# Kernel tuning notes

Hardware: AMD Instinct MI355X
Metric: run time of the kernel (lower is better)

The kernel has to match this reference:

```python
import jax, jax.numpy as jnp
import numpy as np

B, G, C, H, ZD, K, P = 2048, 2000, 50, 256, 32, 10, 4


def _xavier(key, shape, fan_in, fan_out):
    std = (2.0 / (fan_in + fan_out)) ** 0.5
    return std * jax.random.normal(key, shape, dtype=jnp.float32)


def setup_inputs() -> dict:
    key = jax.random.key(0)
    ks = jax.random.split(key, 13)
    X = jax.random.normal(ks[0], (B, G), dtype=jnp.float32)
    M = (jax.random.uniform(ks[1], (C, G)) < 0.1).astype(jnp.float32)
    # backbone: Linear(G,H) + LeakyReLU + Linear(H,H) + LeakyReLU (n_layer_enc=2)
    W1 = _xavier(ks[2], (G, H), G, H)
    b1 = jnp.zeros((H,), dtype=jnp.float32)
    W2 = _xavier(ks[3], (H, H), H, H)
    b2 = jnp.zeros((H,), dtype=jnp.float32)
    # MultiChannelLinear: w [C, ZD, H], b [1, C, ZD] (kaiming-uniform-ish init)
    bound_w = (6.0 / H) ** 0.5
    cw = jax.random.uniform(ks[4], (C, ZD, H), minval=-bound_w, maxval=bound_w, dtype=jnp.float32)
    bound_b = 1.0 / (H ** 0.5)
    cb = jax.random.uniform(ks[5], (1, C, ZD), minval=-bound_b, maxval=bound_b, dtype=jnp.float32)
    prototypes = _xavier(ks[6], (C, K, P, ZD), P * ZD, K)
    logvar = _xavier(ks[7], (C, K, P), P, K)
    c_bias = jnp.zeros((C, K), dtype=jnp.float32)
    bias = jnp.zeros((K,), dtype=jnp.float32)
    importance = _xavier(ks[8], (1, C), C, 1)
    return {"X": X, "M": M, "W1": W1, "b1": b1, "W2": W2, "b2": b2,
            "cw": cw, "cb": cb, "prototypes": prototypes, "logvar": logvar,
            "c_bias": c_bias, "bias": bias, "importance": importance}


def reference(X, M, W1, b1, W2, b2, cw, cb, prototypes, logvar, c_bias, bias, importance):
    # encode: mask input per concept, run shared MLP backbone, per-concept heads
    xm = X[:, None, :] * M[None]                       # [B, C, G]
    h = jax.nn.leaky_relu(jnp.einsum('bcg,gh->bch', xm, W1) + b1)
    h = jax.nn.leaky_relu(jnp.einsum('bch,hk->bck', h, W2) + b2)
    Z = jnp.einsum('bch,coh->bco', h, cw) + cb          # [B, C, ZD]
    # importance scores (dropout p=0 -> identity)
    imp = jnp.abs(importance)                           # [1, C]
    # broadcast squared distance to prototypes: [B, C, K, P]
    diff = Z[:, :, None, None, :] - prototypes[None]
    c2p_dist_sq = jnp.sum(diff * diff, axis=-1)
    scaled = c2p_dist_sq / (2.0 * jnp.exp(logvar))[None]
    c_logits = -jnp.min(scaled, axis=-1) + c_bias[None]  # [B, C, K]
    logits = jnp.log(jnp.sum(jnp.exp(c_logits) * imp[0][None, :, None] + 1e-16, axis=1)) + bias[None]
    return logits, c_logits
```

## Files before the change

### kernel.cpp

```cpp
#include <hip/hip_runtime.h>
#include <hip/hip_bf16.h>

#define NB   2048
#define NG   2000
#define NC   50
#define NH   256
#define NZD  32
#define NK   10
#define NP   4
#define BT   64
#define GS   2048
#define KP   320
#define NCH  10

typedef short short8  __attribute__((ext_vector_type(8)));
typedef short short4v __attribute__((ext_vector_type(4)));
typedef float f32x4   __attribute__((ext_vector_type(4)));
typedef unsigned int uint2v __attribute__((ext_vector_type(2)));

__device__ __forceinline__ unsigned short f2bf(float f) {
    union { float f; unsigned u; } v; v.f = f;
    unsigned r = v.u + 0x7fffu + ((v.u >> 16) & 1u);
    return (unsigned short)(r >> 16);
}

__device__ __forceinline__ unsigned cvt_pk_bf16(float lo, float hi) {
    unsigned r;
    asm("v_cvt_pk_bf16_f32 %0, %1, %2" : "=v"(r) : "v"(lo), "v"(hi));
    return r;
}

__device__ __forceinline__ void gld16(const unsigned short* g, char* l) {
    __builtin_amdgcn_global_load_lds(
        (const __attribute__((address_space(1))) unsigned int*)g,
        (__attribute__((address_space(3))) unsigned int*)l, 16, 0, 0);
}

__global__ void build_gidx(const float* __restrict__ M, int* __restrict__ gidx,
                           int* __restrict__ gcnt) {
    int c = blockIdx.x;
    int t = threadIdx.x;
    __shared__ int wcnt[16];
    __shared__ int base;
    if (t == 0) base = 0;
    __syncthreads();
    for (int g0 = 0; g0 < NG; g0 += 1024) {
        int g = g0 + t;
        bool a = (g < NG) && (M[c * NG + g] != 0.0f);
        unsigned long long mask = __ballot(a);
        int lane = t & 63;
        int w = t >> 6;
        if (lane == 0) wcnt[w] = __popcll(mask);
        int pre = __popcll(mask & ((1ull << lane) - 1ull));
        __syncthreads();
        int woff = base;
        for (int i = 0; i < w; ++i) woff += wcnt[i];
        if (a) gidx[c * GS + woff + pre] = g;
        int tot = 0;
        #pragma unroll
        for (int i = 0; i < 16; ++i) tot += wcnt[i];
        __syncthreads();
        if (t == 0) base += tot;
        __syncthreads();
    }
    if (t == 0) gcnt[c] = base;
}

__global__ void prep_all(const float* __restrict__ X, const float* __restrict__ W1,
                         const float* __restrict__ W2, const float* __restrict__ cw,
                         const int* __restrict__ gidx, const int* __restrict__ gcnt,
                         unsigned short* __restrict__ xt, unsigned short* __restrict__ w1s,
                         unsigned short* __restrict__ w2s, unsigned short* __restrict__ cwb) {
    __shared__ float tile[64][65];
    const int bx = blockIdx.x;
    const int t  = threadIdx.x;
    if (bx < 1024) {
        int gb = bx & 31, bb = bx >> 5;
        int tx = t & 63, tq = t >> 6;
        #pragma unroll
        for (int i = 0; i < 16; ++i) {
            int r = tq * 16 + i;
            int gene = gb * 64 + tx;
            tile[r][tx] = (gene < NG) ? X[(size_t)(bb * 64 + r) * NG + gene] : 0.f;
        }
        __syncthreads();
        #pragma unroll
        for (int i = 0; i < 16; ++i) {
            int gl = tq * 16 + i;
            int gene = gb * 64 + gl;
            if (gene < NG)
                xt[(size_t)gene * NB + bb * 64 + tx] = f2bf(tile[tx][gl]);
        }
    } else if (bx < 1524) {
        int idx = bx - 1024;
        int ch = idx % NCH, c = idx / NCH;
        int col = t;
        int cnt = gcnt[c]; if (cnt > KP) cnt = KP;
        unsigned short v[32];
        #pragma unroll
        for (int kin = 0; kin < 32; ++kin) {
            int k = ch * 32 + kin;
            float x = 0.f;
            if (k < cnt) {
                int g = gidx[c * GS + k];
                x = W1[(size_t)g * NH + col];
            }
            v[kin] = f2bf(x);
        }
        unsigned short* dst = w1s + (((size_t)(c * NCH + ch)) * 256 + col) * 32;
        #pragma unroll
        for (int q = 0; q < 4; ++q) {
            short8 v8;
            #pragma unroll
            for (int i = 0; i < 8; ++i) v8[i] = (short)v[q * 8 + i];
            *(short8*)(dst + (q ^ ((col >> 1) & 3)) * 8) = v8;
        }
    } else if (bx < 1532) {
        int ch = bx - 1524;
        int col = t;
        unsigned short v[32];
        #pragma unroll
        for (int kin = 0; kin < 32; ++kin)
            v[kin] = f2bf(W2[(size_t)(ch * 32 + kin) * NH + col]);
        unsigned short* dst = w2s + ((size_t)ch * 256 + col) * 32;
        #pragma unroll
        for (int q = 0; q < 4; ++q) {
            short8 v8;
            #pragma unroll
            for (int i = 0; i < 8; ++i) v8[i] = (short)v[q * 8 + i];
            *(short8*)(dst + (q ^ ((col >> 1) & 3)) * 8) = v8;
        }
    } else {
        int c = bx - 1532;
        int o = t >> 3, seg = t & 7;
        #pragma unroll
        for (int blk = 0; blk < 4; ++blk) {
            int u = seg * 4 + blk;
            short8 v8;
            #pragma unroll
            for (int i = 0; i < 8; ++i)
                v8[i] = (short)f2bf(cw[((size_t)c * NZD + o) * NH + u * 8 + i]);
            *(short8*)(cwb + (size_t)c * 8192 + o * 256 + (u ^ (o & 7)) * 8) = v8;
        }
    }
}

#define PP_OFF   32768
#define WB0      40960
#define WB1      57344
#define LDS_BYTES 73728

__global__ __launch_bounds__(512, 4) void fused_mfma12(
    const unsigned short* __restrict__ xt,
    const unsigned short* __restrict__ w1s,
    const unsigned short* __restrict__ w2s,
    const unsigned short* __restrict__ cwb,
    const float* __restrict__ b1, const float* __restrict__ b2,
    const float* __restrict__ cb, const float* __restrict__ protos,
    const float* __restrict__ logvar, const float* __restrict__ c_bias,
    const int* __restrict__ gidx, const int* __restrict__ gcnt,
    float* __restrict__ out_cl)
{
    extern __shared__ char sm[];
    const int t  = threadIdx.x;
    const int l  = t & 63;
    const int w  = t >> 6;
    const int lr = l & 15;
    const int lg = l >> 4;
    const int wb = w >> 2;
    const int wh = w & 3;
    const int row0 = blockIdx.x * BT;
    const int c    = blockIdx.y;
    int cnt = gcnt[c]; if (cnt > KP) cnt = KP;
    const int nch = (cnt + 31) >> 5;

    auto Hb = [&](int r, int k) -> char* {
        return sm + r * 512 + ((((k >> 3) ^ (r & 7)) << 4) | ((k & 7) << 1));
    };
    auto XLb = [&](int r, int k) -> char* {
        return sm + r * 640 + ((((k >> 3) ^ (r & 7)) << 4) | ((k & 7) << 1));
    };
    auto stage_w = [&](const unsigned short* gsrc, int base) {
        gld16(gsrc + t * 8,        sm + base + t * 16);
        gld16(gsrc + 4096 + t * 8, sm + base + 8192 + t * 16);
    };
    auto aread = [&](int base, int col, int unit) -> short8 {
        return *(const short8*)(sm + base + col * 64 + ((unit ^ ((col >> 1) & 3)) << 4));
    };

    stage_w(w1s + (size_t)c * NCH * 8192, WB0);

    {
        const int gl2 = t & 63;
        const int rg  = t >> 6;
        short8 xv[5];
        int kk[5];
        #pragma unroll
        for (int i = 0; i < 5; ++i) {
            kk[i] = i * 64 + gl2;
            xv[i] = short8{0,0,0,0,0,0,0,0};
            if (kk[i] < cnt) {
                int g = gidx[c * GS + kk[i]];
                xv[i] = *(const short8*)(xt + (size_t)g * NB + row0 + rg * 8);
            }
        }
        #pragma unroll
        for (int i = 0; i < 5; ++i)
            #pragma unroll
            for (int j = 0; j < 8; ++j)
                *(short*)XLb(rg * 8 + j, kk[i]) = xv[i][j];
    }
    __syncthreads();

    f32x4 acc[2][4];
    #pragma unroll
    for (int nn = 0; nn < 2; ++nn)
        #pragma unroll
        for (int mm = 0; mm < 4; ++mm) acc[nn][mm] = f32x4{0.f, 0.f, 0.f, 0.f};

    for (int ch = 0; ch < nch; ++ch) {
        const int cur = (ch & 1) ? WB1 : WB0;
        const int nxt = (ch & 1) ? WB0 : WB1;
        if (ch + 1 < nch) stage_w(w1s + (size_t)(c * NCH + ch + 1) * 8192, nxt);
        else              stage_w(w2s, nxt);
        short8 a[4], b[2];
        #pragma unroll
        for (int mm = 0; mm < 4; ++mm)
            a[mm] = aread(cur, wh * 64 + mm * 16 + lr, lg);
        #pragma unroll
        for (int nn = 0; nn < 2; ++nn)
            b[nn] = *(const short8*)XLb(wb * 32 + nn * 16 + lr, ch * 32 + lg * 8);
        #pragma unroll
        for (int nn = 0; nn < 2; ++nn)
            #pragma unroll
            for (int mm = 0; mm < 4; ++mm)
                acc[nn][mm] = __builtin_amdgcn_mfma_f32_16x16x32_bf16(a[mm], b[nn], acc[nn][mm], 0, 0, 0);
        __syncthreads();
    }

    #pragma unroll
    for (int mm = 0; mm < 4; ++mm) {
        int k0 = wh * 64 + mm * 16 + lg * 4;
        f32x4 b1v = *(const f32x4*)(b1 + k0);
        #pragma unroll
        for (int nn = 0; nn < 2; ++nn) {
            int r = wb * 32 + nn * 16 + lr;
            float v0 = acc[nn][mm][0] + b1v[0]; v0 = (v0 >= 0.f) ? v0 : 0.01f * v0;
            float v1 = acc[nn][mm][1] + b1v[1]; v1 = (v1 >= 0.f) ? v1 : 0.01f * v1;
            float v2 = acc[nn][mm][2] + b1v[2]; v2 = (v2 >= 0.f) ? v2 : 0.01f * v2;
            float v3 = acc[nn][mm][3] + b1v[3]; v3 = (v3 >= 0.f) ? v3 : 0.01f * v3;
            uint2v pk;
            pk[0] = cvt_pk_bf16(v0, v1);
            pk[1] = cvt_pk_bf16(v2, v3);
            *(uint2v*)Hb(r, k0) = pk;
        }
    }
    __syncthreads();

    f32x4 acc2[2][4];
    #pragma unroll
    for (int nn = 0; nn < 2; ++nn)
        #pragma unroll
        for (int mm = 0; mm < 4; ++mm) acc2[nn][mm] = f32x4{0.f, 0.f, 0.f, 0.f};
    for (int ch2 = 0; ch2 < 8; ++ch2) {
        const int cur = ((nch + ch2) & 1) ? WB1 : WB0;
        const int nxt = ((nch + ch2) & 1) ? WB0 : WB1;
        if (ch2 + 1 < 8) stage_w(w2s + (size_t)(ch2 + 1) * 8192, nxt);
        else             stage_w(cwb + (size_t)c * 8192, nxt);
        short8 a[4], b[2];
        #pragma unroll
        for (int mm = 0; mm < 4; ++mm)
            a[mm] = aread(cur, wh * 64 + mm * 16 + lr, lg);
        #pragma unroll
        for (int nn = 0; nn < 2; ++nn)
            b[nn] = *(const short8*)Hb(wb * 32 + nn * 16 + lr, ch2 * 32 + lg * 8);
        #pragma unroll
        for (int nn = 0; nn < 2; ++nn)
            #pragma unroll
            for (int mm = 0; mm < 4; ++mm)
                acc2[nn][mm] = __builtin_amdgcn_mfma_f32_16x16x32_bf16(a[mm], b[nn], acc2[nn][mm], 0, 0, 0);
        __syncthreads();
    }
    const int cwbase = ((nch + 8) & 1) ? WB1 : WB0;
    const int szbase = ((nch + 8) & 1) ? WB0 : WB1;

    {
        #pragma unroll
        for (int mm = 0; mm < 4; ++mm) {
            int k0 = wh * 64 + mm * 16 + lg * 4;
            f32x4 b2v = *(const f32x4*)(b2 + k0);
            #pragma unroll
            for (int nn = 0; nn < 2; ++nn) {
                int r = wb * 32 + nn * 16 + lr;
                float v0 = acc2[nn][mm][0] + b2v[0]; v0 = (v0 >= 0.f) ? v0 : 0.01f * v0;
                float v1 = acc2[nn][mm][1] + b2v[1]; v1 = (v1 >= 0.f) ? v1 : 0.01f * v1;
                float v2 = acc2[nn][mm][2] + b2v[2]; v2 = (v2 >= 0.f) ? v2 : 0.01f * v2;
                float v3 = acc2[nn][mm][3] + b2v[3]; v3 = (v3 >= 0.f) ? v3 : 0.01f * v3;
                uint2v pk;
                pk[0] = cvt_pk_bf16(v0, v1);
                pk[1] = cvt_pk_bf16(v2, v3);
                *(uint2v*)Hb(r, k0) = pk;
            }
        }
        float* pp = (float*)(sm + PP_OFF);
        for (int i = t; i < NK * NP * NZD; i += 512)
            pp[(i >> 5) * 36 + (i & 31)] = protos[(size_t)c * (NK * NP * NZD) + i];
        if (t < NK * NP) pp[1440 + t] = 0.5f * expf(-logvar[c * (NK * NP) + t]);
        if (t < NK)      pp[1480 + t] = c_bias[c * NK + t];
    }
    __syncthreads();

    {
        const int rt = w & 3, ot = w >> 2;
        const int o = ot * 16 + lr;
        f32x4 az = f32x4{0.f, 0.f, 0.f, 0.f};
        #pragma unroll
        for (int ch = 0; ch < 8; ++ch) {
            short8 afr = *(const short8*)(sm + cwbase + o * 512 +
                                          ((((ch << 2) + lg) ^ (o & 7)) << 4));
            short8 bfr = *(const short8*)Hb(rt * 16 + lr, ch * 32 + lg * 8);
            az = __builtin_amdgcn_mfma_f32_16x16x32_bf16(afr, bfr, az, 0, 0, 0);
        }
        f32x4 cb4 = *(const f32x4*)(cb + c * NZD + ot * 16 + lg * 4);
        float* SZ = (float*)(sm + szbase);
        #pragma unroll
        for (int i = 0; i < 4; ++i)
            SZ[(rt * 16 + lr) * 36 + ot * 16 + lg * 4 + i] = az[i] + cb4[i];
    }
    __syncthreads();

    {
        const float* SZ  = (const float*)(sm + szbase);
        const float* pp  = (const float*)(sm + PP_OFF);
        const float* i2e = pp + 1440;
        const float* cbs = pp + 1480;
        const int rloc = (w & 3) * 16 + lr;
        f32x4 z[8];
        #pragma unroll
        for (int j = 0; j < 8; ++j)
            z[j] = *(const f32x4*)(SZ + rloc * 36 + j * 4);
        const int kk0 = (w >> 2) * 5;
        #pragma unroll
        for (int kk = kk0; kk < kk0 + 5; ++kk) {
            int kp = kk * NP + lg;
            f32x4 d = f32x4{0.f, 0.f, 0.f, 0.f};
            #pragma unroll
            for (int j = 0; j < 8; ++j) {
                f32x4 p = *(const f32x4*)(pp + kp * 36 + j * 4);
                f32x4 df = z[j] - p;
                d += df * df;
            }
            float sc = ((d[0] + d[1]) + (d[2] + d[3])) * i2e[kp];
            sc = fminf(sc, __shfl_xor(sc, 16));
            sc = fminf(sc, __shfl_xor(sc, 32));
            if (lg == 0)
                out_cl[((size_t)(row0 + rloc) * NC + c) * NK + kk] = cbs[kk] - sc;
        }
    }
}

__global__ __launch_bounds__(256, 1) void fused_main(
    const float* __restrict__ X,  const float* __restrict__ W1,
    const float* __restrict__ b1, const float* __restrict__ W2,
    const float* __restrict__ b2, const float* __restrict__ cw,
    const float* __restrict__ cb, const float* __restrict__ protos,
    const float* __restrict__ logvar, const float* __restrict__ c_bias,
    const int* __restrict__ gidx, const int* __restrict__ gcnt,
    float* __restrict__ out_cl)
{
    extern __shared__ float smemf[];
    float (*sh_big)[258] = (float (*)[258])smemf;
    float (*sh_w)[258]   = (float (*)[258])(smemf + 16512);
    float (*sh_x)[33]    = (float (*)[33])(smemf + 16512 + 8256);
    int*  sh_gid         = (int*)(smemf + 16512 + 8256 + 2112);

    const int t   = threadIdx.x;
    const int tx  = t & 15;
    const int ty  = t >> 4;
    const int row0 = blockIdx.x * 64;
    const int c    = blockIdx.y;

    float acc[4][16];
    #pragma unroll
    for (int i = 0; i < 4; ++i)
        #pragma unroll
        for (int l = 0; l < 16; ++l) acc[i][l] = 0.f;

    const int cnt = gcnt[c];
    const int nch = (cnt + 31) >> 5;
    for (int ch = 0; ch < nch; ++ch) {
        __syncthreads();
        if (t < 32) {
            int gi = ch * 32 + t;
            sh_gid[t] = (gi < cnt) ? gidx[c * GS + gi] : -1;
        }
        __syncthreads();
        #pragma unroll 4
        for (int jj = 0; jj < 32; ++jj) {
            int g = sh_gid[jj];
            sh_w[jj][t] = (g >= 0) ? W1[g * NH + t] : 0.f;
        }
        {
            int j  = t & 31;
            int rb2 = (t >> 5) * 8;
            int g  = sh_gid[j];
            #pragma unroll
            for (int ii = 0; ii < 8; ++ii)
                sh_x[rb2 + ii][j] = (g >= 0) ? X[(size_t)(row0 + rb2 + ii) * NG + g] : 0.f;
        }
        __syncthreads();
        #pragma unroll 8
        for (int j = 0; j < 32; ++j) {
            float xv[4];
            #pragma unroll
            for (int i = 0; i < 4; ++i) xv[i] = sh_x[ty * 4 + i][j];
            #pragma unroll
            for (int l = 0; l < 16; ++l) {
                float wv = sh_w[j][l * 16 + tx];
                #pragma unroll
                for (int i = 0; i < 4; ++i) acc[i][l] = fmaf(xv[i], wv, acc[i][l]);
            }
        }
    }
    #pragma unroll
    for (int i = 0; i < 4; ++i)
        #pragma unroll
        for (int l = 0; l < 16; ++l) {
            int col = l * 16 + tx;
            float v = acc[i][l] + b1[col];
            sh_big[ty * 4 + i][col] = (v >= 0.f) ? v : 0.01f * v;
        }

    float acc2[4][16];
    #pragma unroll
    for (int i = 0; i < 4; ++i)
        #pragma unroll
        for (int l = 0; l < 16; ++l) acc2[i][l] = 0.f;
    for (int ch = 0; ch < NH / 32; ++ch) {
        __syncthreads();
        #pragma unroll 4
        for (int jj = 0; jj < 32; ++jj)
            sh_w[jj][t] = W2[(size_t)(ch * 32 + jj) * NH + t];
        __syncthreads();
        #pragma unroll 8
        for (int j = 0; j < 32; ++j) {
            float xv[4];
            #pragma unroll
            for (int i = 0; i < 4; ++i) xv[i] = sh_big[ty * 4 + i][ch * 32 + j];
            #pragma unroll
            for (int l = 0; l < 16; ++l) {
                float wv = sh_w[j][l * 16 + tx];
                #pragma unroll
                for (int i = 0; i < 4; ++i) acc2[i][l] = fmaf(xv[i], wv, acc2[i][l]);
            }
        }
    }
    __syncthreads();
    #pragma unroll
    for (int i = 0; i < 4; ++i)
        #pragma unroll
        for (int l = 0; l < 16; ++l) {
            int col = l * 16 + tx;
            float v = acc2[i][l] + b2[col];
            sh_big[ty * 4 + i][col] = (v >= 0.f) ? v : 0.01f * v;
        }
    #pragma unroll 4
    for (int o = 0; o < NZD; ++o)
        sh_w[o][t] = cw[((size_t)c * NZD + o) * NH + t];
    __syncthreads();
    {
        int o  = t & 31;
        int rg = t >> 5;
        float cbv = cb[c * NZD + o];
        float zv[8];
        #pragma unroll
        for (int i = 0; i < 8; ++i) zv[i] = cbv;
        for (int h = 0; h < NH; ++h) {
            float wv = sh_w[o][h];
            #pragma unroll
            for (int i = 0; i < 8; ++i)
                zv[i] = fmaf(sh_big[rg * 8 + i][h], wv, zv[i]);
        }
        #pragma unroll
        for (int i = 0; i < 8; ++i) sh_x[rg * 8 + i][o] = zv[i];
    }
    __syncthreads();
    float* proto_s = &sh_w[0][0];
    float* i2e_s   = proto_s + NK * NP * NZD;
    float* cbias_s = i2e_s + NK * NP;
    for (int i = t; i < NK * NP * NZD; i += 256)
        proto_s[i] = protos[(size_t)c * NK * NP * NZD + i];
    if (t < NK * NP) i2e_s[t] = 0.5f * expf(-logvar[c * NK * NP + t]);
    if (t < NK)      cbias_s[t] = c_bias[c * NK + t];
    __syncthreads();
    for (int task = t; task < 64 * NK; task += 256) {
        int r = task / NK;
        int k = task - r * NK;
        float best = 3.4e38f;
        #pragma unroll
        for (int p = 0; p < NP; ++p) {
            float d2 = 0.f;
            const float* ppr = proto_s + (k * NP + p) * NZD;
            #pragma unroll
            for (int o = 0; o < NZD; ++o) {
                float dv = sh_x[r][o] - ppr[o];
                d2 = fmaf(dv, dv, d2);
            }
            float sc = d2 * i2e_s[k * NP + p];
            best = fminf(best, sc);
        }
        out_cl[((size_t)(row0 + r) * NC + c) * NK + k] = cbias_s[k] - best;
    }
}

__global__ void reduce_logits(const float* __restrict__ cl,
                              const float* __restrict__ importance,
                              const float* __restrict__ bias,
                              float* __restrict__ out) {
    int idx = blockIdx.x * blockDim.x + threadIdx.x;
    if (idx >= NB * NK) return;
    int b = idx / NK;
    int k = idx - b * NK;
    float s = 0.f;
    #pragma unroll
    for (int c = 0; c < NC; ++c) {
        float imp = fabsf(importance[c]);
        s += expf(cl[((size_t)b * NC + c) * NK + k]) * imp + 1e-16f;
    }
    out[idx] = logf(s) + bias[k];
}

extern "C" void kernel_launch(void* const* d_in, const int* in_sizes, int n_in,
                              void* d_out, int out_size, void* d_ws, size_t ws_size,
                              hipStream_t stream) {
    const float* X      = (const float*)d_in[0];
    const float* M      = (const float*)d_in[1];
    const float* W1     = (const float*)d_in[2];
    const float* b1     = (const float*)d_in[3];
    const float* W2     = (const float*)d_in[4];
    const float* b2     = (const float*)d_in[5];
    const float* cw     = (const float*)d_in[6];
    const float* cb     = (const float*)d_in[7];
    const float* protos = (const float*)d_in[8];
    const float* logvar = (const float*)d_in[9];
    const float* c_bias = (const float*)d_in[10];
    const float* bias   = (const float*)d_in[11];
    const float* imp    = (const float*)d_in[12];

    float* out_logits = (float*)d_out;
    float* out_cl     = out_logits + NB * NK;

    const size_t o_gcnt = (size_t)NC * GS * 4;
    const size_t o_w1s  = o_gcnt + 256;
    const size_t o_w2s  = o_w1s + (size_t)NC * NCH * 256 * 32 * 2;
    const size_t o_cwb  = o_w2s + (size_t)8 * 256 * 32 * 2;
    const size_t o_xt   = o_cwb + (size_t)NC * 32 * 256 * 2;
    const size_t need   = o_xt + (size_t)NG * NB * 2;

    int* gidx = (int*)d_ws;
    int* gcnt = (int*)((char*)d_ws + o_gcnt);
    unsigned short* w1s = (unsigned short*)((char*)d_ws + o_w1s);
    unsigned short* w2s = (unsigned short*)((char*)d_ws + o_w2s);
    unsigned short* cwb = (unsigned short*)((char*)d_ws + o_cwb);
    unsigned short* xt  = (unsigned short*)((char*)d_ws + o_xt);

    build_gidx<<<NC, 1024, 0, stream>>>(M, gidx, gcnt);

    if (ws_size >= need) {
        prep_all<<<1582, 256, 0, stream>>>(X, W1, W2, cw, gidx, gcnt, xt, w1s, w2s, cwb);
        fused_mfma12<<<dim3(NB / BT, NC), 512, LDS_BYTES, stream>>>(
            xt, w1s, w2s, cwb, b1, b2, cb, protos, logvar, c_bias, gidx, gcnt, out_cl);
    } else {
        size_t smem = (size_t)(16512 + 8256 + 2112) * 4 + 32 * 4;
        fused_main<<<dim3(NB / 64, NC), 256, smem, stream>>>(
            X, W1, b1, W2, b2, cw, cb, protos, logvar, c_bias, gidx, gcnt, out_cl);
    }
    reduce_logits<<<(NB * NK + 255) / 256, 256, 0, stream>>>(out_cl, imp, bias, out_logits);
}
```

Measured before the change: 86.79 us.

## Prefetch weight chunks two steps ahead with explicit vmcnt waits and barriers

Restructures the fused MLP kernel's weight streaming so each loop iteration issues the load for chunk j+2 after the compute barrier. It waits with s_waitcnt vmcnt(2) instead of a full __syncthreads, so global-to-LDS loads stay in flight across iterations. Bias vectors are also hoisted into registers at kernel start. This aims to hide global load latency behind the MFMA work, at the cost of two barriers per chunk and hand-written waitcnt logic that depends on the exact count of outstanding loads.

```diff
diff --git a/kernel.cpp b/kernel.cpp
--- a/kernel.cpp
+++ b/kernel.cpp
@@ -150,7 +150,7 @@
 #define WB1      57344
 #define LDS_BYTES 73728
 
-__global__ __launch_bounds__(512, 4) void fused_mfma12(
+__global__ __launch_bounds__(512, 4) void fused_mfma13(
     const unsigned short* __restrict__ xt,
     const unsigned short* __restrict__ w1s,
     const unsigned short* __restrict__ w2s,
@@ -180,15 +180,30 @@
     auto XLb = [&](int r, int k) -> char* {
         return sm + r * 640 + ((((k >> 3) ^ (r & 7)) << 4) | ((k & 7) << 1));
     };
-    auto stage_w = [&](const unsigned short* gsrc, int base) {
-        gld16(gsrc + t * 8,        sm + base + t * 16);
-        gld16(gsrc + 4096 + t * 8, sm + base + 8192 + t * 16);
+    auto gsrc = [&](int j) -> const unsigned short* {
+        if (j < nch)     return w1s + ((size_t)(c * NCH + j)) * 8192;
+        if (j < nch + 8) return w2s + (size_t)(j - nch) * 8192;
+        return cwb + (size_t)c * 8192;
+    };
+    auto stage_j = [&](int j) {
+        const unsigned short* g = gsrc(j);
+        char* base = sm + ((j & 1) ? WB1 : WB0);
+        gld16(g + t * 8,        base + t * 16);
+        gld16(g + 4096 + t * 8, base + 8192 + t * 16);
     };
     auto aread = [&](int base, int col, int unit) -> short8 {
         return *(const short8*)(sm + base + col * 64 + ((unit ^ ((col >> 1) & 3)) << 4));
     };
 
-    stage_w(w1s + (size_t)c * NCH * 8192, WB0);
+    f32x4 b1v[4], b2v[4];
+    #pragma unroll
+    for (int mm = 0; mm < 4; ++mm) {
+        int k0 = wh * 64 + mm * 16 + lg * 4;
+        b1v[mm] = *(const f32x4*)(b1 + k0);
+        b2v[mm] = *(const f32x4*)(b2 + k0);
+    }
+    stage_j(0);
+    stage_j(1);
 
     {
         const int gl2 = t & 63;
@@ -210,7 +225,9 @@
             for (int j = 0; j < 8; ++j)
                 *(short*)XLb(rg * 8 + j, kk[i]) = xv[i][j];
     }
-    __syncthreads();
+    asm volatile("s_waitcnt lgkmcnt(0)" ::: "memory");
+    __builtin_amdgcn_s_barrier();
+    asm volatile("" ::: "memory");
 
     f32x4 acc[2][4];
     #pragma unroll
@@ -218,68 +235,76 @@
         #pragma unroll
         for (int mm = 0; mm < 4; ++mm) acc[nn][mm] = f32x4{0.f, 0.f, 0.f, 0.f};
 
-    for (int ch = 0; ch < nch; ++ch) {
-        const int cur = (ch & 1) ? WB1 : WB0;
-        const int nxt = (ch & 1) ? WB0 : WB1;
-        if (ch + 1 < nch) stage_w(w1s + (size_t)(c * NCH + ch + 1) * 8192, nxt);
-        else              stage_w(w2s, nxt);
+    for (int j = 0; j < nch; ++j) {
+        asm volatile("s_waitcnt vmcnt(2)" ::: "memory");
+        __builtin_amdgcn_s_barrier();
+        asm volatile("" ::: "memory");
+        const int cur = (j & 1) ? WB1 : WB0;
         short8 a[4], b[2];
         #pragma unroll
         for (int mm = 0; mm < 4; ++mm)
             a[mm] = aread(cur, wh * 64 + mm * 16 + lr, lg);
         #pragma unroll
         for (int nn = 0; nn < 2; ++nn)
-            b[nn] = *(const short8*)XLb(wb * 32 + nn * 16 + lr, ch * 32 + lg * 8);
+            b[nn] = *(const short8*)XLb(wb * 32 + nn * 16 + lr, j * 32 + lg * 8);
         #pragma unroll
         for (int nn = 0; nn < 2; ++nn)
             #pragma unroll
             for (int mm = 0; mm < 4; ++mm)
                 acc[nn][mm] = __builtin_amdgcn_mfma_f32_16x16x32_bf16(a[mm], b[nn], acc[nn][mm], 0, 0, 0);
-        __syncthreads();
+        asm volatile("s_waitcnt lgkmcnt(0)" ::: "memory");
+        __builtin_amdgcn_s_barrier();
+        asm volatile("" ::: "memory");
+        stage_j(j + 2);
     }
 
     #pragma unroll
     for (int mm = 0; mm < 4; ++mm) {
-        int k0 = wh * 64 + mm * 16 + lg * 4;
-        f32x4 b1v = *(const f32x4*)(b1 + k0);
         #pragma unroll
         for (int nn = 0; nn < 2; ++nn) {
+            int k0 = wh * 64 + mm * 16 + lg * 4;
             int r = wb * 32 + nn * 16 + lr;
-            float v0 = acc[nn][mm][0] + b1v[0]; v0 = (v0 >= 0.f) ? v0 : 0.01f * v0;
-            float v1 = acc[nn][mm][1] + b1v[1]; v1 = (v1 >= 0.f) ? v1 : 0.01f * v1;
-            float v2 = acc[nn][mm][2] + b1v[2]; v2 = (v2 >= 0.f) ? v2 : 0.01f * v2;
-            float v3 = acc[nn][mm][3] + b1v[3]; v3 = (v3 >= 0.f) ? v3 : 0.01f * v3;
+            float v0 = acc[nn][mm][0] + b1v[mm][0]; v0 = (v0 >= 0.f) ? v0 : 0.01f * v0;
+            float v1 = acc[nn][mm][1] + b1v[mm][1]; v1 = (v1 >= 0.f) ? v1 : 0.01f * v1;
+            float v2 = acc[nn][mm][2] + b1v[mm][2]; v2 = (v2 >= 0.f) ? v2 : 0.01f * v2;
+            float v3 = acc[nn][mm][3] + b1v[mm][3]; v3 = (v3 >= 0.f) ? v3 : 0.01f * v3;
             uint2v pk;
             pk[0] = cvt_pk_bf16(v0, v1);
             pk[1] = cvt_pk_bf16(v2, v3);
             *(uint2v*)Hb(r, k0) = pk;
         }
     }
-    __syncthreads();
+    asm volatile("s_waitcnt lgkmcnt(0)" ::: "memory");
+    __builtin_amdgcn_s_barrier();
+    asm volatile("" ::: "memory");
 
     f32x4 acc2[2][4];
     #pragma unroll
     for (int nn = 0; nn < 2; ++nn)
         #pragma unroll
         for (int mm = 0; mm < 4; ++mm) acc2[nn][mm] = f32x4{0.f, 0.f, 0.f, 0.f};
-    for (int ch2 = 0; ch2 < 8; ++ch2) {
-        const int cur = ((nch + ch2) & 1) ? WB1 : WB0;
-        const int nxt = ((nch + ch2) & 1) ? WB0 : WB1;
-        if (ch2 + 1 < 8) stage_w(w2s + (size_t)(ch2 + 1) * 8192, nxt);
-        else             stage_w(cwb + (size_t)c * 8192, nxt);
+    for (int j = nch; j < nch + 8; ++j) {
+        asm volatile("s_waitcnt vmcnt(2)" ::: "memory");
+        __builtin_amdgcn_s_barrier();
+        asm volatile("" ::: "memory");
+        const int cur = (j & 1) ? WB1 : WB0;
+        const int ch = j - nch;
         short8 a[4], b[2];
         #pragma unroll
         for (int mm = 0; mm < 4; ++mm)
             a[mm] = aread(cur, wh * 64 + mm * 16 + lr, lg);
         #pragma unroll
         for (int nn = 0; nn < 2; ++nn)
-            b[nn] = *(const short8*)Hb(wb * 32 + nn * 16 + lr, ch2 * 32 + lg * 8);
+            b[nn] = *(const short8*)Hb(wb * 32 + nn * 16 + lr, ch * 32 + lg * 8);
         #pragma unroll
         for (int nn = 0; nn < 2; ++nn)
             #pragma unroll
             for (int mm = 0; mm < 4; ++mm)
                 acc2[nn][mm] = __builtin_amdgcn_mfma_f32_16x16x32_bf16(a[mm], b[nn], acc2[nn][mm], 0, 0, 0);
-        __syncthreads();
+        asm volatile("s_waitcnt lgkmcnt(0)" ::: "memory");
+        __builtin_amdgcn_s_barrier();
+        asm volatile("" ::: "memory");
+        if (j + 2 <= nch + 8) stage_j(j + 2);
     }
     const int cwbase = ((nch + 8) & 1) ? WB1 : WB0;
     const int szbase = ((nch + 8) & 1) ? WB0 : WB1;
@@ -287,15 +312,14 @@
     {
         #pragma unroll
         for (int mm = 0; mm < 4; ++mm) {
-            int k0 = wh * 64 + mm * 16 + lg * 4;
-            f32x4 b2v = *(const f32x4*)(b2 + k0);
             #pragma unroll
             for (int nn = 0; nn < 2; ++nn) {
+                int k0 = wh * 64 + mm * 16 + lg * 4;
                 int r = wb * 32 + nn * 16 + lr;
-                float v0 = acc2[nn][mm][0] + b2v[0]; v0 = (v0 >= 0.f) ? v0 : 0.01f * v0;
-                float v1 = acc2[nn][mm][1] + b2v[1]; v1 = (v1 >= 0.f) ? v1 : 0.01f * v1;
-                float v2 = acc2[nn][mm][2] + b2v[2]; v2 = (v2 >= 0.f) ? v2 : 0.01f * v2;
-                float v3 = acc2[nn][mm][3] + b2v[3]; v3 = (v3 >= 0.f) ? v3 : 0.01f * v3;
+                float v0 = acc2[nn][mm][0] + b2v[mm][0]; v0 = (v0 >= 0.f) ? v0 : 0.01f * v0;
+                float v1 = acc2[nn][mm][1] + b2v[mm][1]; v1 = (v1 >= 0.f) ? v1 : 0.01f * v1;
+                float v2 = acc2[nn][mm][2] + b2v[mm][2]; v2 = (v2 >= 0.f) ? v2 : 0.01f * v2;
+                float v3 = acc2[nn][mm][3] + b2v[mm][3]; v3 = (v3 >= 0.f) ? v3 : 0.01f * v3;
                 uint2v pk;
                 pk[0] = cvt_pk_bf16(v0, v1);
                 pk[1] = cvt_pk_bf16(v2, v3);
@@ -568,7 +592,7 @@
 
     if (ws_size >= need) {
         prep_all<<<1582, 256, 0, stream>>>(X, W1, W2, cw, gidx, gcnt, xt, w1s, w2s, cwb);
-        fused_mfma12<<<dim3(NB / BT, NC), 512, LDS_BYTES, stream>>>(
+        fused_mfma13<<<dim3(NB / BT, NC), 512, LDS_BYTES, stream>>>(
             xt, w1s, w2s, cwb, b1, b2, cb, protos, logvar, c_bias, gidx, gcnt, out_cl);
     } else {
         size_t smem = (size_t)(16512 + 8256 + 2112) * 4 + 32 * 4;
```

New measurement: 83.87 us. -3.4%, faster.
